# Performance work log

Hardware: AMD Instinct MI355X
Metric: run time of the kernel (lower is better)

Reference implementation:

```python
import jax, jax.numpy as jnp
import numpy as np

VOCAB = 32000
DIM = 1024
HID = 4096
MAXLEN = 2048
NH = 2       # number of sequential LowRankLinearAttention layers
KD = 64      # key_dim hardcoded in the module
B = 2
L = 2048


def setup_inputs() -> dict:
    key = jax.random.key(0)
    ks = jax.random.split(key, 12)
    def rn(k, shape, scale):
        return jax.random.normal(k, shape, dtype=jnp.float32) * scale
    return {
        "input_indices": jax.random.randint(ks[0], (B, L), 0, VOCAB),
        "token_embed": rn(ks[1], (VOCAB, DIM), 0.02),
        "pos_embed": rn(ks[2], (MAXLEN, DIM), 0.02),
        # per-layer attention projections (stored [in, out]; x @ W == torch Linear)
        "Wq": rn(ks[3], (NH, DIM, KD), DIM ** -0.5),
        "Wk": rn(ks[4], (NH, DIM, KD), DIM ** -0.5),
        "Wv": rn(ks[5], (NH, DIM, KD), DIM ** -0.5),
        "Wo": rn(ks[6], (NH, KD, DIM), KD ** -0.5),
        "norm_g": jnp.ones((NH, DIM), jnp.float32),
        "norm_b": jnp.zeros((NH, DIM), jnp.float32),
        "out_norm_g": jnp.ones((DIM,), jnp.float32),
        "out_norm_b": jnp.zeros((DIM,), jnp.float32),
        "W1": rn(ks[7], (DIM, HID), DIM ** -0.5),
        "b1": jnp.zeros((HID,), jnp.float32),
        "W2": rn(ks[8], (HID, VOCAB), HID ** -0.5),
        "b2": jnp.zeros((VOCAB,), jnp.float32),
    }


def _layernorm(x, g, b, eps=1e-5):
    m = jnp.mean(x, axis=-1, keepdims=True)
    v = jnp.var(x, axis=-1, keepdims=True)
    return (x - m) / jnp.sqrt(v + eps) * g + b


def _lowrank_linear_attn(x, Wq, Wk, Wv, Wo):
    # x: [B,L,D]; Q,K,V: [B,L,k]
    Q = jax.nn.elu(x @ Wq) + 1.0
    K = jax.nn.elu(x @ Wk) + 1.0
    V = x @ Wv
    # causal prefix sums of outer products K_t V_t^T -> [B,L,k,k]
    KV_sum = jnp.cumsum(K[..., :, None] * V[..., None, :], axis=1)
    K_sum = jnp.cumsum(K, axis=1)
    num = jnp.einsum('blk,blkj->blj', Q, KV_sum)          # [B,L,k]
    den = jnp.einsum('blk,blk->bl', Q, K_sum)[..., None]  # [B,L,1]
    return (num / (den + 1e-6)) @ Wo


def reference(input_indices, token_embed, pos_embed, Wq, Wk, Wv, Wo,
              norm_g, norm_b, out_norm_g, out_norm_b, W1, b1, W2, b2):
    seq_len = input_indices.shape[1]
    x = token_embed[input_indices] + pos_embed[jnp.arange(seq_len)]
    for i in range(Wq.shape[0]):
        x = x + _lowrank_linear_attn(x, Wq[i], Wk[i], Wv[i], Wo[i])
        x = _layernorm(x, norm_g[i], norm_b[i])
    x = _layernorm(x, out_norm_g, out_norm_b)
    h = jax.nn.gelu(x @ W1 + b1, approximate=False)  # torch nn.GELU default = erf
    logits = h @ W2 + b2
    return logits
```

## Files before the change

kernel.cpp:

```cpp
#include <hip/hip_runtime.h>

typedef __attribute__((ext_vector_type(4))) float  f4;
typedef __attribute__((ext_vector_type(2))) float  f2;
typedef __attribute__((ext_vector_type(4))) unsigned short us4;
typedef __attribute__((ext_vector_type(8))) short  s8;
typedef __attribute__((ext_vector_type(4))) float  f32x4;

__device__ __forceinline__ unsigned short f2bf(float f) {
  unsigned u = __float_as_uint(f);
  u += 0x7fffu + ((u >> 16) & 1u);
  return (unsigned short)(u >> 16);
}
__device__ __forceinline__ float elu1(float x) { return x > 0.f ? x + 1.f : __expf(x); }
__device__ __forceinline__ float gelu_erf(float x) { return 0.5f * x * (1.f + erff(x * 0.70710678118654752f)); }

__device__ __forceinline__ void async16(const void* g, void* l) {
  __builtin_amdgcn_global_load_lds((const __attribute__((address_space(1))) void*)g,
                                   (__attribute__((address_space(3))) void*)l, 16, 0, 0);
}

__global__ __launch_bounds__(256) void embed_kernel(
    const int* __restrict__ idx, const float* __restrict__ tok,
    const float* __restrict__ pos, float* __restrict__ X, unsigned short* __restrict__ XB)
{
  int g = blockIdx.x * 256 + threadIdx.x;
  int t = g >> 8;
  int c4 = (g & 255) * 4;
  int l = t & 2047;
  int tk = idx[t];
  f4 v = *(const f4*)(tok + (size_t)tk * 1024 + c4);
  f4 p = *(const f4*)(pos + (size_t)l * 1024 + c4);
  v += p;
  *(f4*)(X + (size_t)t * 1024 + c4) = v;
  us4 o = { f2bf(v[0]), f2bf(v[1]), f2bf(v[2]), f2bf(v[3]) };
  *(us4*)(XB + (size_t)t * 1024 + c4) = o;
}

__global__ __launch_bounds__(256) void transpose_cvt(
    const float* __restrict__ src, unsigned short* __restrict__ dst, int N, int K)
{
  __shared__ unsigned short t[64][72];
  int k0 = blockIdx.x * 64, n0 = blockIdx.y * 64;
  int tid = threadIdx.x;
#pragma unroll
  for (int i = 0; i < 4; ++i) {
    int f = tid + i * 256;
    int r = f >> 4, c4 = (f & 15) * 4;
    f4 v = *(const f4*)(src + (size_t)(k0 + r) * N + n0 + c4);
    us4 o = { f2bf(v[0]), f2bf(v[1]), f2bf(v[2]), f2bf(v[3]) };
    *(us4*)&t[r][c4] = o;
  }
  __syncthreads();
#pragma unroll
  for (int i = 0; i < 4; ++i) {
    int f = tid + i * 256;
    int nr = f >> 4, kc4 = (f & 15) * 4;
    us4 o = { t[kc4 + 0][nr], t[kc4 + 1][nr], t[kc4 + 2][nr], t[kc4 + 3][nr] };
    *(us4*)(dst + (size_t)(n0 + nr) * K + k0 + kc4) = o;
  }
}

template<int EPI, int BF32>
__global__ __launch_bounds__(256) void gemm_bt(
    const unsigned short* __restrict__ A, const unsigned short* __restrict__ Bt,
    const float* __restrict__ Bf, const float* __restrict__ bias,
    void* __restrict__ Cv, int M, int N, int K, int mtiles)
{
  __shared__ unsigned short As[128 * 32];
  __shared__ unsigned short Bs[128 * 32];
  int bid = blockIdx.x;
  int mt = bid % mtiles, nt = bid / mtiles;
  int m0 = mt * 128, n0 = nt * 128;
  int tid = threadIdx.x, lane = tid & 63, w = tid >> 6;
  int wm = (w & 1) * 64, wn = (w >> 1) * 64;

  int c0 = w * 128 + lane, c1 = c0 + 64;
  size_t aO0 = (size_t)(m0 + (c0 >> 2)) * K + (size_t)((c0 & 3) * 8);
  size_t aO1 = (size_t)(m0 + (c1 >> 2)) * K + (size_t)((c1 & 3) * 8);
  size_t bO0 = (size_t)(n0 + (c0 >> 2)) * K + (size_t)((c0 & 3) * 8);
  size_t bO1 = (size_t)(n0 + (c1 >> 2)) * K + (size_t)((c1 & 3) * 8);
  unsigned short* lA0 = As + (w * 128) * 8;
  unsigned short* lA1 = As + (w * 128 + 64) * 8;
  unsigned short* lB0 = Bs + (w * 128) * 8;
  unsigned short* lB1 = Bs + (w * 128 + 64) * 8;

  f32x4 acc[4][4];
  f32x4 zz = {0.f, 0.f, 0.f, 0.f};
#pragma unroll
  for (int i = 0; i < 4; ++i)
#pragma unroll
    for (int j = 0; j < 4; ++j) acc[i][j] = zz;

  int rr = lane & 15, kh = (lane >> 4) * 8;
  const unsigned short* Ar = As + (wm + rr) * 32 + kh;
  const unsigned short* Br = Bs + (wn + rr) * 32 + kh;

  for (int k0 = 0; k0 < K; k0 += 32) {
    async16(A + aO0 + k0, lA0);
    async16(A + aO1 + k0, lA1);
    if constexpr (!BF32) {
      async16(Bt + bO0 + k0, lB0);
      async16(Bt + bO1 + k0, lB1);
    } else {
#pragma unroll
      for (int i = 0; i < 4; ++i) {
        int f = tid + i * 256;
        int kr = f >> 5, c4 = (f & 31) * 4;
        f4 v = *(const f4*)(Bf + (size_t)(k0 + kr) * N + n0 + c4);
#pragma unroll
        for (int e = 0; e < 4; ++e) Bs[(c4 + e) * 32 + kr] = f2bf(v[e]);
      }
    }
    __syncthreads();
    s8 af[4], bfr[4];
#pragma unroll
    for (int mi = 0; mi < 4; ++mi) af[mi] = *(const s8*)(Ar + mi * 512);
#pragma unroll
    for (int ni = 0; ni < 4; ++ni) bfr[ni] = *(const s8*)(Br + ni * 512);
#pragma unroll
    for (int mi = 0; mi < 4; ++mi)
#pragma unroll
      for (int ni = 0; ni < 4; ++ni)
        acc[mi][ni] = __builtin_amdgcn_mfma_f32_16x16x32_bf16(af[mi], bfr[ni], acc[mi][ni], 0, 0, 0);
    __syncthreads();
  }

  int cr = (lane >> 4) * 4;
#pragma unroll
  for (int mi = 0; mi < 4; ++mi) {
#pragma unroll
    for (int ni = 0; ni < 4; ++ni) {
      int gc = n0 + wn + ni * 16 + rr;
      float bv = (EPI > 0) ? bias[gc] : 0.f;
#pragma unroll
      for (int r = 0; r < 4; ++r) {
        int gr = m0 + wm + mi * 16 + cr + r;
        float v = acc[mi][ni][r] + bv;
        if constexpr (EPI == 1) {
          ((unsigned short*)Cv)[(size_t)gr * N + gc] = f2bf(gelu_erf(v));
        } else {
          ((float*)Cv)[(size_t)gr * N + gc] = v;
        }
      }
    }
  }
}

template<int KB, int NH, int READA, int WAITV, typename STG>
__device__ __forceinline__ void phase_fn(const char* Ab, const char* Bb,
                                         s8 (&af)[8], f32x4 (&acc)[8][4], STG stg)
{
  s8 bf0 = *(const s8*)(Bb + ((NH * 2 + 0) * 2 + KB) * 1024);
  s8 bf1 = *(const s8*)(Bb + ((NH * 2 + 1) * 2 + KB) * 1024);
  if constexpr (READA) {
#pragma unroll
    for (int f = 0; f < 8; ++f)
      af[f] = *(const s8*)(Ab + (f * 2 + KB) * 1024);
  }
  stg();
  __builtin_amdgcn_s_barrier();
  asm volatile("s_waitcnt lgkmcnt(0)" ::: "memory");
  __builtin_amdgcn_sched_barrier(0);
  __builtin_amdgcn_s_setprio(1);
#pragma unroll
  for (int f = 0; f < 8; ++f) {
    acc[f][NH * 2 + 0] =
        __builtin_amdgcn_mfma_f32_16x16x32_bf16(af[f], bf0, acc[f][NH * 2 + 0], 0, 0, 0);
    acc[f][NH * 2 + 1] =
        __builtin_amdgcn_mfma_f32_16x16x32_bf16(af[f], bf1, acc[f][NH * 2 + 1], 0, 0, 0);
  }
  __builtin_amdgcn_s_setprio(0);
  if constexpr (WAITV) asm volatile("s_waitcnt vmcnt(8)" ::: "memory");
  __builtin_amdgcn_s_barrier();
}

template<int EPI>
__global__ __launch_bounds__(512) void gemm256(
    const unsigned short* __restrict__ A, const unsigned short* __restrict__ Bt,
    const float* __restrict__ bias, void* __restrict__ Cv,
    int M, int N, int K, int mtiles)
{
  __shared__ __align__(16) char smem[131072];
  char* A0r = smem;
  char* B0r = smem + 32768;
  char* A1r = smem + 65536;
  char* B1r = smem + 98304;

  const int tid = threadIdx.x, lane = tid & 63, w = tid >> 6;
  const int wm = w >> 2, wn = w & 3;
  const int NT = K >> 6;

  int nwg = gridDim.x, orig = blockIdx.x;
  int q = nwg >> 3, r = nwg & 7;
  int xcd = orig & 7, lin = orig >> 3;
  int swz = (xcd < r ? xcd * (q + 1) : r * (q + 1) + (xcd - r) * q) + lin;
  int mt = swz % mtiles, nt = swz / mtiles;
  int m0 = mt * 256, n0 = nt * 256;

  const size_t klane8 = (size_t)((lane >> 4) << 3);
  const size_t arow0 = (size_t)(m0 + w * 32 + (lane & 15)) * K;
  const size_t arow1 = arow0 + (size_t)16 * K;
  const size_t brow0 = (size_t)(n0 + w * 32 + (lane & 15)) * K;
  const size_t brow1 = brow0 + (size_t)16 * K;
  const int stgoff = w * 4096;

  auto stgA = [&](char* reg, int kt, int kb) {
    int ktc = kt < NT ? kt : NT - 1;
    size_t kk = (size_t)ktc * 64 + (size_t)(kb * 32) + klane8;
    char* d = reg + stgoff + kb * 1024;
    async16(A + arow0 + kk, d);
    async16(A + arow1 + kk, d + 2048);
  };
  auto stgB = [&](char* reg, int kt, int kb) {
    int ktc = kt < NT ? kt : NT - 1;
    size_t kk = (size_t)ktc * 64 + (size_t)(kb * 32) + klane8;
    char* d = reg + stgoff + kb * 1024;
    async16(Bt + brow0 + kk, d);
    async16(Bt + brow1 + kk, d + 2048);
  };

  const char* Ab0 = A0r + wm * 16384 + lane * 16;
  const char* Bb0 = B0r + wn * 8192 + lane * 16;
  const char* Ab1 = A1r + wm * 16384 + lane * 16;
  const char* Bb1 = B1r + wn * 8192 + lane * 16;

  f32x4 acc[8][4];
  f32x4 zz = {0.f, 0.f, 0.f, 0.f};
#pragma unroll
  for (int i = 0; i < 8; ++i)
#pragma unroll
    for (int j = 0; j < 4; ++j) acc[i][j] = zz;
  s8 af[8];

  stgA(A0r, 0, 0); stgB(B0r, 0, 0);
  stgA(A0r, 0, 1); stgB(B0r, 0, 1);
  stgA(A1r, 1, 0); stgB(B1r, 1, 0);
  asm volatile("s_waitcnt vmcnt(8)" ::: "memory");
  __builtin_amdgcn_s_barrier();

  for (int te = 0; te < NT; te += 2) {
    phase_fn<0, 0, 1, 0>(Ab0, Bb0, af, acc, [&] { stgA(A1r, te + 1, 1); });
    phase_fn<0, 1, 0, 1>(Ab0, Bb0, af, acc, [&] { stgB(B1r, te + 1, 1); });
    phase_fn<1, 1, 1, 0>(Ab0, Bb0, af, acc, [&] { stgA(A0r, te + 2, 0); });
    phase_fn<1, 0, 0, 1>(Ab0, Bb0, af, acc, [&] { stgB(B0r, te + 2, 0); });
    phase_fn<0, 0, 1, 0>(Ab1, Bb1, af, acc, [&] { stgA(A0r, te + 2, 1); });
    phase_fn<0, 1, 0, 1>(Ab1, Bb1, af, acc, [&] { stgB(B0r, te + 2, 1); });
    phase_fn<1, 1, 1, 0>(Ab1, Bb1, af, acc, [&] { stgA(A1r, te + 3, 0); });
    phase_fn<1, 0, 0, 1>(Ab1, Bb1, af, acc, [&] { stgB(B1r, te + 3, 0); });
  }

  int rr = lane & 15, cr = (lane >> 4) * 4;
#pragma unroll
  for (int f = 0; f < 8; ++f) {
#pragma unroll
    for (int ni = 0; ni < 4; ++ni) {
      int gc = n0 + wn * 64 + ni * 16 + rr;
      float bv = bias[gc];
#pragma unroll
      for (int rg = 0; rg < 4; ++rg) {
        int gr = m0 + wm * 128 + f * 16 + cr + rg;
        float v = acc[f][ni][rg] + bv;
        if constexpr (EPI == 1) {
          ((unsigned short*)Cv)[(size_t)gr * N + gc] = f2bf(gelu_erf(v));
        } else {
          ((float*)Cv)[(size_t)gr * N + gc] = v;
        }
      }
    }
  }
}

__global__ __launch_bounds__(256) void chunk_sums(
    const float* __restrict__ QKV, float* __restrict__ KVc, float* __restrict__ Ksum)
{
  __shared__ float Ks[64][68], Vs[64][68];
  int blk = blockIdx.x, t0 = blk * 64, tid = threadIdx.x;
#pragma unroll
  for (int i = 0; i < 4; ++i) {
    int f = tid + i * 256;
    int r = f >> 4, c4 = (f & 15) * 4;
    const float* s = QKV + (size_t)(t0 + r) * 256;
    f4 k = *(const f4*)(s + 64 + c4);
    f4 v = *(const f4*)(s + 128 + c4);
#pragma unroll
    for (int e = 0; e < 4; ++e) { Ks[r][c4 + e] = elu1(k[e]); Vs[r][c4 + e] = v[e]; }
  }
  __syncthreads();
  int i0 = tid >> 2, jb = (tid & 3) * 16;
  f4 a0 = {0,0,0,0}, a1 = {0,0,0,0}, a2 = {0,0,0,0}, a3 = {0,0,0,0};
  for (int t = 0; t < 64; ++t) {
    float kk = Ks[t][i0];
    a0 += kk * (*(const f4*)&Vs[t][jb]);
    a1 += kk * (*(const f4*)&Vs[t][jb + 4]);
    a2 += kk * (*(const f4*)&Vs[t][jb + 8]);
    a3 += kk * (*(const f4*)&Vs[t][jb + 12]);
  }
  float* d = KVc + (size_t)blk * 4096 + i0 * 64 + jb;
  *(f4*)(d) = a0; *(f4*)(d + 4) = a1; *(f4*)(d + 8) = a2; *(f4*)(d + 12) = a3;
  if (tid < 64) {
    float s = 0.f;
    for (int t = 0; t < 64; ++t) s += Ks[t][tid];
    Ksum[(size_t)blk * 64 + tid] = s;
  }
}

__global__ __launch_bounds__(256) void prefix_state(
    const float* __restrict__ KVc, const float* __restrict__ Ksum,
    float* __restrict__ KVp, float* __restrict__ Ksump)
{
  int b = blockIdx.x >> 3, seg = blockIdx.x & 7;
  int e = seg * 512 + threadIdx.x * 2;
  f2 run = {0.f, 0.f};
#pragma unroll
  for (int c = 0; c < 32; ++c) {
    size_t base = ((size_t)b * 32 + c) * 4096 + e;
    *(f2*)(KVp + base) = run;
    run += *(const f2*)(KVc + base);
  }
  if (seg == 0 && threadIdx.x < 64) {
    float rs = 0.f; int i = threadIdx.x;
#pragma unroll
    for (int c = 0; c < 32; ++c) {
      size_t base = ((size_t)b * 32 + c) * 64 + i;
      Ksump[base] = rs;
      rs += Ksum[base];
    }
  }
}

__global__ __launch_bounds__(256) void attn_ns(
    const float* __restrict__ QKV, const float* __restrict__ KVp,
    const float* __restrict__ Ksump, float* __restrict__ NsG)
{
  __shared__ float Qs[64][68], Ks[64][68], Vs[64][68], Ss[64][68], Ps[64][68];
  __shared__ float ksps[64];
  int blk = blockIdx.x, t0 = blk * 64, tid = threadIdx.x;
#pragma unroll
  for (int i = 0; i < 4; ++i) {
    int f = tid + i * 256;
    int r = f >> 4, c4 = (f & 15) * 4;
    const float* s = QKV + (size_t)(t0 + r) * 256;
    f4 q = *(const f4*)(s + c4);
    f4 k = *(const f4*)(s + 64 + c4);
    f4 v = *(const f4*)(s + 128 + c4);
    f4 p = *(const f4*)(KVp + (size_t)blk * 4096 + r * 64 + c4);
#pragma unroll
    for (int e = 0; e < 4; ++e) {
      Qs[r][c4 + e] = elu1(q[e]); Ks[r][c4 + e] = elu1(k[e]);
      Vs[r][c4 + e] = v[e];       Ps[r][c4 + e] = p[e];
    }
  }
  if (tid < 64) ksps[tid] = Ksump[(size_t)blk * 64 + tid];
  __syncthreads();
  int tq = tid >> 2, jb = (tid & 3) * 16;
#pragma unroll
  for (int jj = 0; jj < 16; ++jj) {
    int tk = jb + jj;
    float s = 0.f;
    if (tk <= tq) {
#pragma unroll
      for (int k4 = 0; k4 < 16; ++k4) {
        f4 q = *(const f4*)&Qs[tq][k4 * 4];
        f4 k = *(const f4*)&Ks[tk][k4 * 4];
        s += q[0] * k[0] + q[1] * k[1] + q[2] * k[2] + q[3] * k[3];
      }
    }
    Ss[tq][tk] = s;
  }
  __syncthreads();
  f4 a0 = {0,0,0,0}, a1 = {0,0,0,0}, a2 = {0,0,0,0}, a3 = {0,0,0,0};
  for (int t = 0; t < 64; ++t) {
    float s = Ss[tq][t];
    a0 += s * (*(const f4*)&Vs[t][jb]);
    a1 += s * (*(const f4*)&Vs[t][jb + 4]);
    a2 += s * (*(const f4*)&Vs[t][jb + 8]);
    a3 += s * (*(const f4*)&Vs[t][jb + 12]);
  }
  for (int k = 0; k < 64; ++k) {
    float q = Qs[tq][k];
    a0 += q * (*(const f4*)&Ps[k][jb]);
    a1 += q * (*(const f4*)&Ps[k][jb + 4]);
    a2 += q * (*(const f4*)&Ps[k][jb + 8]);
    a3 += q * (*(const f4*)&Ps[k][jb + 12]);
  }
  float den = 0.f;
  for (int t = 0; t < 64; ++t) den += Ss[tq][t];
  for (int k = 0; k < 64; ++k) den += Qs[tq][k] * ksps[k];
  float inv = 1.f / (den + 1e-6f);
  float* d = NsG + (size_t)(t0 + tq) * 64 + jb;
  *(f4*)(d)      = a0 * inv;
  *(f4*)(d + 4)  = a1 * inv;
  *(f4*)(d + 8)  = a2 * inv;
  *(f4*)(d + 12) = a3 * inv;
}

__global__ __launch_bounds__(256) void attn_apply(
    const float* __restrict__ NsG, const float* __restrict__ Wo, float* __restrict__ X)
{
  __shared__ float Ns[64][68];
  __shared__ float Wt[64][260];
  int chunk = blockIdx.x >> 2, dg = blockIdx.x & 3;
  int t0 = chunk * 64, d0 = dg * 256, tid = threadIdx.x;
#pragma unroll
  for (int i = 0; i < 4; ++i) {
    int f = tid + i * 256;
    int r = f >> 4, c4 = (f & 15) * 4;
    *(f4*)&Ns[r][c4] = *(const f4*)(NsG + (size_t)(t0 + r) * 64 + c4);
  }
#pragma unroll
  for (int i = 0; i < 16; ++i) {
    int f = tid + i * 256;
    int r = f >> 6, c4 = (f & 63) * 4;
    *(f4*)&Wt[r][c4] = *(const f4*)(Wo + (size_t)r * 1024 + d0 + c4);
  }
  __syncthreads();
  int w = tid >> 6, lane = tid & 63;
  for (int ts = 0; ts < 16; ++ts) {
    int t = w * 16 + ts;
    float a0 = 0.f, a1 = 0.f, a2 = 0.f, a3 = 0.f;
#pragma unroll
    for (int j = 0; j < 64; ++j) {
      float nv = Ns[t][j];
      a0 += nv * Wt[j][lane];
      a1 += nv * Wt[j][64 + lane];
      a2 += nv * Wt[j][128 + lane];
      a3 += nv * Wt[j][192 + lane];
    }
    size_t o = (size_t)(t0 + t) * 1024 + d0 + lane;
    X[o]       += a0;
    X[o + 64]  += a1;
    X[o + 128] += a2;
    X[o + 192] += a3;
  }
}

__global__ __launch_bounds__(256) void layernorm_kernel(
    float* __restrict__ X, unsigned short* __restrict__ XB,
    const float* __restrict__ g, const float* __restrict__ b)
{
  int t = blockIdx.x * 4 + (threadIdx.x >> 6);
  int lane = threadIdx.x & 63;
  float* row = X + (size_t)t * 1024;
  f4 v[4];
  float s = 0.f, s2 = 0.f;
#pragma unroll
  for (int i = 0; i < 4; ++i) {
    v[i] = *(const f4*)(row + (i * 64 + lane) * 4);
#pragma unroll
    for (int e = 0; e < 4; ++e) { s += v[i][e]; s2 += v[i][e] * v[i][e]; }
  }
#pragma unroll
  for (int off = 32; off > 0; off >>= 1) {
    s  += __shfl_xor(s, off, 64);
    s2 += __shfl_xor(s2, off, 64);
  }
  float mean = s * (1.f / 1024.f);
  float var = s2 * (1.f / 1024.f) - mean * mean;
  float rstd = rsqrtf(var + 1e-5f);
#pragma unroll
  for (int i = 0; i < 4; ++i) {
    int d = (i * 64 + lane) * 4;
    f4 gv = *(const f4*)(g + d);
    f4 bv = *(const f4*)(b + d);
    f4 y;
#pragma unroll
    for (int e = 0; e < 4; ++e) y[e] = (v[i][e] - mean) * rstd * gv[e] + bv[e];
    *(f4*)(row + d) = y;
    us4 o = { f2bf(y[0]), f2bf(y[1]), f2bf(y[2]), f2bf(y[3]) };
    *(us4*)(XB + (size_t)t * 1024 + d) = o;
  }
}

extern "C" void kernel_launch(void* const* d_in, const int* in_sizes, int n_in,
                              void* d_out, int out_size, void* d_ws, size_t ws_size,
                              hipStream_t stream) {
  (void)in_sizes; (void)n_in; (void)out_size;
  const int*   idx = (const int*)d_in[0];
  const float* tok = (const float*)d_in[1];
  const float* pos = (const float*)d_in[2];
  const float* Wq  = (const float*)d_in[3];
  const float* Wk  = (const float*)d_in[4];
  const float* Wv  = (const float*)d_in[5];
  const float* Wo  = (const float*)d_in[6];
  const float* ng  = (const float*)d_in[7];
  const float* nb  = (const float*)d_in[8];
  const float* ong = (const float*)d_in[9];
  const float* onb = (const float*)d_in[10];
  const float* W1  = (const float*)d_in[11];
  const float* b1  = (const float*)d_in[12];
  const float* W2  = (const float*)d_in[13];
  const float* b2  = (const float*)d_in[14];
  float* out = (float*)d_out;
  char* ws = (char*)d_ws;

  float* X            = (float*)(ws + 0);
  unsigned short* XB  = (unsigned short*)(ws + 16777216);
  unsigned short* QT0 = (unsigned short*)(ws + 25165824);
  unsigned short* QT1 = (unsigned short*)(ws + 25690112);
  float* QKVB         = (float*)(ws + 26214400);
  float* KVC          = (float*)(ws + 30408704);
  float* KSUM         = (float*)(ws + 31457280);
  float* KVP          = (float*)(ws + 31490048);
  float* KSP          = (float*)(ws + 32538624);
  unsigned short* W1T = (unsigned short*)(ws + 32571392);
  unsigned short* H   = (unsigned short*)(ws + 40960000);
  unsigned short* W2T = (unsigned short*)(ws + 74514432);
  float* NSG = KVC;
  bool bigws = ws_size >= 336658432ull;

  hipMemsetAsync(QT0, 0, 524288, stream);
  hipMemsetAsync(QT1, 0, 524288, stream);
  transpose_cvt<<<dim3(16, 1), 256, 0, stream>>>(Wq,          QT0,              64, 1024);
  transpose_cvt<<<dim3(16, 1), 256, 0, stream>>>(Wk,          QT0 + 64 * 1024,  64, 1024);
  transpose_cvt<<<dim3(16, 1), 256, 0, stream>>>(Wv,          QT0 + 128 * 1024, 64, 1024);
  transpose_cvt<<<dim3(16, 1), 256, 0, stream>>>(Wq + 65536,  QT1,              64, 1024);
  transpose_cvt<<<dim3(16, 1), 256, 0, stream>>>(Wk + 65536,  QT1 + 64 * 1024,  64, 1024);
  transpose_cvt<<<dim3(16, 1), 256, 0, stream>>>(Wv + 65536,  QT1 + 128 * 1024, 64, 1024);
  transpose_cvt<<<dim3(16, 64), 256, 0, stream>>>(W1, W1T, 4096, 1024);
  if (bigws)
    transpose_cvt<<<dim3(64, 500), 256, 0, stream>>>(W2, W2T, 32000, 4096);

  embed_kernel<<<4096, 256, 0, stream>>>(idx, tok, pos, X, XB);

  for (int layer = 0; layer < 2; ++layer) {
    const unsigned short* QT = layer ? QT1 : QT0;
    gemm_bt<0, 0><<<64, 256, 0, stream>>>(XB, QT, nullptr, nullptr, QKVB, 4096, 256, 1024, 32);
    chunk_sums<<<64, 256, 0, stream>>>(QKVB, KVC, KSUM);
    prefix_state<<<16, 256, 0, stream>>>(KVC, KSUM, KVP, KSP);
    attn_ns<<<64, 256, 0, stream>>>(QKVB, KVP, KSP, NSG);
    attn_apply<<<256, 256, 0, stream>>>(NSG, Wo + (size_t)layer * 65536, X);
    layernorm_kernel<<<1024, 256, 0, stream>>>(X, XB, ng + layer * 1024, nb + layer * 1024);
  }
  layernorm_kernel<<<1024, 256, 0, stream>>>(X, XB, ong, onb);

  gemm256<1><<<256, 512, 0, stream>>>(XB, W1T, b1, H, 4096, 4096, 1024, 16);
  if (bigws)
    gemm256<2><<<2000, 512, 0, stream>>>(H, W2T, b2, out, 4096, 32000, 4096, 16);
  else
    gemm_bt<2, 1><<<8000, 256, 0, stream>>>(H, nullptr, W2, b2, out, 4096, 32000, 4096, 32);
}
```

Baseline: 1.660 ms.

## Software-pipeline LDS fragment reads one phase ahead of MFMAs in gemm256

Restructures the gemm256 main loop so that each phase issues the LDS reads for the next phase's A/B fragments into double-buffered registers while its MFMAs consume the fragments loaded earlier. The second barrier per phase is removed, and waits become partial lgkmcnt/vmcnt counts. It also sets launch_bounds(512,2), which asks for two workgroups per CU. The cost is more register pressure from the doubled fragment buffers, and the reduced synchronisation risks LDS read/write hazards if the wait counts or buffer ordering are wrong.

```diff
diff --git a/kernel.cpp b/kernel.cpp
--- a/kernel.cpp
+++ b/kernel.cpp
@@ -146,36 +146,40 @@
   }
 }
 
-template<int KB, int NH, int READA, int WAITV, typename STG>
-__device__ __forceinline__ void phase_fn(const char* Ab, const char* Bb,
-                                         s8 (&af)[8], f32x4 (&acc)[8][4], STG stg)
-{
-  s8 bf0 = *(const s8*)(Bb + ((NH * 2 + 0) * 2 + KB) * 1024);
-  s8 bf1 = *(const s8*)(Bb + ((NH * 2 + 1) * 2 + KB) * 1024);
-  if constexpr (READA) {
+template<int RA, int RDKB, int RDNH, int ACCN, int LGN, typename STG>
+__device__ __forceinline__ void phaseX(
+    const char* ArdB, const char* BrdB,
+    s8 (&afDst)[8], s8 (&bfDst)[2],
+    const s8 (&afUse)[8], const s8 (&bfUse)[2],
+    f32x4 (&acc)[8][4], STG stg)
+{
+  if constexpr (RA) {
 #pragma unroll
     for (int f = 0; f < 8; ++f)
-      af[f] = *(const s8*)(Ab + (f * 2 + KB) * 1024);
-  }
+      afDst[f] = *(const s8*)(ArdB + (f * 2 + RDKB) * 1024);
+  }
+  bfDst[0] = *(const s8*)(BrdB + ((RDNH * 2 + 0) * 2 + RDKB) * 1024);
+  bfDst[1] = *(const s8*)(BrdB + ((RDNH * 2 + 1) * 2 + RDKB) * 1024);
   stg();
+  asm volatile("s_waitcnt vmcnt(6)" ::: "memory");
   __builtin_amdgcn_s_barrier();
-  asm volatile("s_waitcnt lgkmcnt(0)" ::: "memory");
+  if constexpr (LGN == 2) asm volatile("s_waitcnt lgkmcnt(2)" ::: "memory");
+  else                    asm volatile("s_waitcnt lgkmcnt(10)" ::: "memory");
   __builtin_amdgcn_sched_barrier(0);
   __builtin_amdgcn_s_setprio(1);
 #pragma unroll
   for (int f = 0; f < 8; ++f) {
-    acc[f][NH * 2 + 0] =
-        __builtin_amdgcn_mfma_f32_16x16x32_bf16(af[f], bf0, acc[f][NH * 2 + 0], 0, 0, 0);
-    acc[f][NH * 2 + 1] =
-        __builtin_amdgcn_mfma_f32_16x16x32_bf16(af[f], bf1, acc[f][NH * 2 + 1], 0, 0, 0);
+    acc[f][ACCN * 2 + 0] =
+        __builtin_amdgcn_mfma_f32_16x16x32_bf16(afUse[f], bfUse[0], acc[f][ACCN * 2 + 0], 0, 0, 0);
+    acc[f][ACCN * 2 + 1] =
+        __builtin_amdgcn_mfma_f32_16x16x32_bf16(afUse[f], bfUse[1], acc[f][ACCN * 2 + 1], 0, 0, 0);
   }
   __builtin_amdgcn_s_setprio(0);
-  if constexpr (WAITV) asm volatile("s_waitcnt vmcnt(8)" ::: "memory");
-  __builtin_amdgcn_s_barrier();
+  __builtin_amdgcn_sched_barrier(0);
 }
 
 template<int EPI>
-__global__ __launch_bounds__(512) void gemm256(
+__global__ __launch_bounds__(512, 2) void gemm256(
     const unsigned short* __restrict__ A, const unsigned short* __restrict__ Bt,
     const float* __restrict__ bias, void* __restrict__ Cv,
     int M, int N, int K, int mtiles)
@@ -230,23 +234,27 @@
   for (int i = 0; i < 8; ++i)
 #pragma unroll
     for (int j = 0; j < 4; ++j) acc[i][j] = zz;
-  s8 af[8];
+  s8 afA[8], afB[8], bfA[2], bfB[2];
 
   stgA(A0r, 0, 0); stgB(B0r, 0, 0);
   stgA(A0r, 0, 1); stgB(B0r, 0, 1);
   stgA(A1r, 1, 0); stgB(B1r, 1, 0);
   asm volatile("s_waitcnt vmcnt(8)" ::: "memory");
   __builtin_amdgcn_s_barrier();
+#pragma unroll
+  for (int f = 0; f < 8; ++f) afA[f] = *(const s8*)(Ab0 + (f * 2) * 1024);
+  bfA[0] = *(const s8*)(Bb0 + 0);
+  bfA[1] = *(const s8*)(Bb0 + 2048);
 
   for (int te = 0; te < NT; te += 2) {
-    phase_fn<0, 0, 1, 0>(Ab0, Bb0, af, acc, [&] { stgA(A1r, te + 1, 1); });
-    phase_fn<0, 1, 0, 1>(Ab0, Bb0, af, acc, [&] { stgB(B1r, te + 1, 1); });
-    phase_fn<1, 1, 1, 0>(Ab0, Bb0, af, acc, [&] { stgA(A0r, te + 2, 0); });
-    phase_fn<1, 0, 0, 1>(Ab0, Bb0, af, acc, [&] { stgB(B0r, te + 2, 0); });
-    phase_fn<0, 0, 1, 0>(Ab1, Bb1, af, acc, [&] { stgA(A0r, te + 2, 1); });
-    phase_fn<0, 1, 0, 1>(Ab1, Bb1, af, acc, [&] { stgB(B0r, te + 2, 1); });
-    phase_fn<1, 1, 1, 0>(Ab1, Bb1, af, acc, [&] { stgA(A1r, te + 3, 0); });
-    phase_fn<1, 0, 0, 1>(Ab1, Bb1, af, acc, [&] { stgB(B1r, te + 3, 0); });
+    phaseX<0, 0, 1, 0,  2>(Ab0, Bb0, afA, bfB, afA, bfA, acc, [&] { stgA(A1r, te + 1, 1); });
+    phaseX<1, 1, 1, 1, 10>(Ab0, Bb0, afB, bfA, afA, bfB, acc, [&] { stgB(B1r, te + 1, 1); });
+    phaseX<0, 1, 0, 1,  2>(Ab0, Bb0, afA, bfB, afB, bfA, acc, [&] { stgA(A0r, te + 2, 0); });
+    phaseX<1, 0, 0, 0, 10>(Ab1, Bb1, afA, bfA, afB, bfB, acc, [&] { stgB(B0r, te + 2, 0); });
+    phaseX<0, 0, 1, 0,  2>(Ab1, Bb1, afA, bfB, afA, bfA, acc, [&] { stgA(A0r, te + 2, 1); });
+    phaseX<1, 1, 1, 1, 10>(Ab1, Bb1, afB, bfA, afA, bfB, acc, [&] { stgB(B0r, te + 2, 1); });
+    phaseX<0, 1, 0, 1,  2>(Ab1, Bb1, afA, bfB, afB, bfA, acc, [&] { stgA(A1r, te + 3, 0); });
+    phaseX<1, 0, 0, 0, 10>(Ab0, Bb0, afA, bfA, afB, bfB, acc, [&] { stgB(B1r, te + 3, 0); });
   }
 
   int rr = lane & 15, cr = (lane >> 4) * 4;
```

Result: no change. 1.661 ms (+0.1%).
